# Performance work log

Measured on AMD Instinct MI355X. Metric: run time of the kernel, lower is better.

Reference implementation:

```python
import jax, jax.numpy as jnp
import numpy as np

EMBED_DIM = 768
HEADS = 8
HEAD_DIM = 128  # gnn_hidden_dim
OUT_DIM = HEADS * HEAD_DIM  # 1024, concat=True
NEG_SLOPE = 0.2  # PyG GATConv leaky_relu slope


def setup_inputs() -> dict:
    key = jax.random.key(0)
    ks = jax.random.split(key, 12)
    N, E = 10000, 160000
    x = jax.random.normal(ks[0], (N, EMBED_DIM), dtype=jnp.float32)
    edge_index = jax.random.randint(ks[1], (2, E), 0, N, dtype=jnp.int32)
    edge_attr = jax.random.uniform(ks[2], (E, 1), dtype=jnp.float32)
    # GATConv params (single layer, edge_dim=1)
    sc = 1.0 / np.sqrt(EMBED_DIM)
    W = jax.random.normal(ks[3], (EMBED_DIM, OUT_DIM), dtype=jnp.float32) * sc
    att_src = jax.random.normal(ks[4], (HEADS, HEAD_DIM), dtype=jnp.float32) * 0.1
    att_dst = jax.random.normal(ks[5], (HEADS, HEAD_DIM), dtype=jnp.float32) * 0.1
    W_edge = jax.random.normal(ks[6], (1, OUT_DIM), dtype=jnp.float32)
    att_edge = jax.random.normal(ks[7], (HEADS, HEAD_DIM), dtype=jnp.float32) * 0.1
    bias = jnp.zeros((OUT_DIM,), dtype=jnp.float32)
    # final classifier: in = 3*OUT_DIM (global pool + text node + image node)
    clf_W = jax.random.normal(ks[8], (3 * OUT_DIM, 2), dtype=jnp.float32) * (1.0 / np.sqrt(3 * OUT_DIM))
    clf_b = jnp.zeros((2,), dtype=jnp.float32)
    return {
        'x': x, 'edge_index': edge_index, 'edge_attr': edge_attr,
        'text_idx': 0, 'image_idx': 1,
        'W': W, 'att_src': att_src, 'att_dst': att_dst,
        'W_edge': W_edge, 'att_edge': att_edge, 'bias': bias,
        'clf_W': clf_W, 'clf_b': clf_b,
    }


def gat_layer(x, edge_index, edge_attr, W, att_src, att_dst, W_edge, att_edge, bias):
    N = x.shape[0]
    # add self-loops with edge_attr = mean of existing edge_attr (PyG default fill_value='mean')
    loop = jnp.arange(N, dtype=edge_index.dtype)
    ei = jnp.concatenate([edge_index, jnp.stack([loop, loop])], axis=1)
    ea_mean = jnp.mean(edge_attr, axis=0, keepdims=True)
    ea = jnp.concatenate([edge_attr, jnp.broadcast_to(ea_mean, (N, edge_attr.shape[1]))], axis=0)
    src, dst = ei[0], ei[1]
    xs = (x @ W).reshape(N, HEADS, HEAD_DIM)             # [N, H, C]
    a_src = jnp.einsum('nhc,hc->nh', xs, att_src)        # per-node src logits
    a_dst = jnp.einsum('nhc,hc->nh', xs, att_dst)
    e_emb = (ea @ W_edge).reshape(-1, HEADS, HEAD_DIM)   # [Etot, H, C]
    a_edge = jnp.einsum('ehc,hc->eh', e_emb, att_edge)
    alpha = jax.nn.leaky_relu(a_src[src] + a_dst[dst] + a_edge, NEG_SLOPE)  # [Etot, H]
    # softmax over incoming edges of each dst node
    m = jax.ops.segment_max(alpha, dst, num_segments=N)
    ex = jnp.exp(alpha - m[dst])
    denom = jax.ops.segment_sum(ex, dst, num_segments=N)
    w = ex / denom[dst]                                  # normalized attention [Etot, H]
    msg = xs[src] * w[:, :, None]                        # [Etot, H, C]
    out = jax.ops.segment_sum(msg, dst, num_segments=N)  # [N, H, C]
    return out.reshape(N, OUT_DIM) + bias


def reference(x, edge_index, edge_attr, text_idx, image_idx,
              W, att_src, att_dst, W_edge, att_edge, bias, clf_W, clf_b):
    # single GAT layer (num_gat_layers=1 -> no ELU/dropout after, eval mode)
    h = gat_layer(x, edge_index, edge_attr, W, att_src, att_dst, W_edge, att_edge, bias)
    g = jnp.mean(h, axis=0, keepdims=True)               # global_mean_pool, batch=None
    t = h[text_idx][None, :]
    im = h[image_idx][None, :]
    fused = jnp.concatenate([g, t, im], axis=1)          # [1, 3*OUT_DIM]
    logits = fused @ clf_W + clf_b                       # [1, 2]
    return logits
```

## Files before the change

### kernel.cpp

```cpp
#include <hip/hip_runtime.h>

#define NN 10000
#define EE 160000
#define ETOT (EE + NN)
#define EMB 768
#define ODIM 1024
#define NEG 0.2f
#define CAP 56

#define OFF_P      0
#define OFF_Q      12288
#define OFF_EAACC  12296
#define OFF_CNTD   12304
#define OFF_CNTS   22304
#define ZERO_START 12296
#define ZERO_CNT   20008
#define OFF_A      32304
#define OFF_SRCD   192304
#define OFF_DSTS   752304
#define OFF_PACK   1312304
#define OFF_EXD    1482304
#define OFF_EXS    5962304
#define OFF_RDEN   10442304
#define OFF_S      10522304
#define OFF_Z      10602304
#define OFF_YPART  10614592

__global__ __launch_bounds__(256) void k1f(
    const float* __restrict__ W, const float* __restrict__ att_src,
    const float* __restrict__ att_dst, const float* __restrict__ W_edge,
    const float* __restrict__ att_edge, const float* __restrict__ edge_attr,
    const int* __restrict__ ei, float* __restrict__ ws) {
  int b = blockIdx.x;
  if (b < 48) {
    int tid = b * 256 + threadIdx.x;
    int k = tid >> 4, j = tid & 15, h = j & 7;
    const float* att = (j < 8) ? att_src : att_dst;
    const float* wp = W + k * ODIM + h * 128;
    const float* ap = att + h * 128;
    float acc = 0.f;
    #pragma unroll 8
    for (int c = 0; c < 128; ++c) acc += wp[c] * ap[c];
    ws[OFF_P + k * 16 + j] = acc;
  } else if (b == 48) {
    if (threadIdx.x < 8) {
      int h = threadIdx.x;
      float acc = 0.f;
      #pragma unroll 8
      for (int c = 0; c < 128; ++c) acc += W_edge[h * 128 + c] * att_edge[h * 128 + c];
      ws[OFF_Q + h] = acc;
    }
  } else if (b < 113) {
    int bi = b - 49;
    float acc = 0.f;
    for (int i = bi * 256 + threadIdx.x; i < EE; i += 64 * 256) acc += edge_attr[i];
    #pragma unroll
    for (int off = 32; off > 0; off >>= 1) acc += __shfl_down(acc, off, 64);
    if ((threadIdx.x & 63) == 0) atomicAdd(&ws[OFF_EAACC], acc);
  } else {
    int e = (b - 113) * 256 + threadIdx.x;
    if (e >= ETOT) return;
    int src, dst;
    if (e < EE) { src = ei[e]; dst = ei[EE + e]; } else { src = dst = e - EE; }
    int* cntd = (int*)(ws + OFF_CNTD);
    int* cnts = (int*)(ws + OFF_CNTS);
    int pd = atomicAdd(&cntd[dst], 1);
    if (pd < CAP) ((int*)(ws + OFF_SRCD))[dst * CAP + pd] = src;
    int ps = atomicAdd(&cnts[src], 1);
    if (ps < CAP) ((int*)(ws + OFF_DSTS))[src * CAP + ps] = dst;
    if (pd > CAP) pd = CAP;
    if (ps > CAP) ps = CAP;
    ((int*)(ws + OFF_PACK))[e] = pd | (ps << 16);
  }
}

__global__ __launch_bounds__(256) void kAx(const float* __restrict__ x,
                                           float* __restrict__ ws) {
  __shared__ float smem[12288];
  for (int i = threadIdx.x; i < 3072; i += 256)
    ((float4*)smem)[i] = ((const float4*)(ws + OFF_P))[i];
  __syncthreads();
  int nl = threadIdx.x & 31, cg = threadIdx.x >> 5;
  int n = blockIdx.x * 32 + nl;
  float a[16];
  #pragma unroll
  for (int j = 0; j < 16; ++j) a[j] = 0.f;
  if (n < NN) {
    const float4* xr = (const float4*)(x + n * EMB + cg * 96);
    for (int kk = 0; kk < 24; ++kk) {
      float4 xv = xr[kk];
      const float* pr = &smem[(cg * 96 + kk * 4) * 16];
      #pragma unroll
      for (int j = 0; j < 16; ++j) a[j] += xv.x * pr[j];
      #pragma unroll
      for (int j = 0; j < 16; ++j) a[j] += xv.y * pr[16 + j];
      #pragma unroll
      for (int j = 0; j < 16; ++j) a[j] += xv.z * pr[32 + j];
      #pragma unroll
      for (int j = 0; j < 16; ++j) a[j] += xv.w * pr[48 + j];
    }
  }
  __syncthreads();
  #pragma unroll
  for (int j = 0; j < 16; ++j) smem[(cg * 16 + j) * 33 + nl] = a[j];
  __syncthreads();
  for (int w = threadIdx.x; w < 512; w += 256) {
    int rnl = w >> 4, j = w & 15;
    int nn = blockIdx.x * 32 + rnl;
    if (nn < NN) {
      float s = 0.f;
      #pragma unroll
      for (int c2 = 0; c2 < 8; ++c2) s += smem[(c2 * 16 + j) * 33 + rnl];
      ws[OFF_A + nn * 16 + j] = s;
    }
  }
}

__global__ __launch_bounds__(128) void kE(const int* __restrict__ ei,
                                          const float* __restrict__ edge_attr,
                                          const float* __restrict__ bias,
                                          const float* __restrict__ clf_W,
                                          const float* __restrict__ clf_b,
                                          float* __restrict__ out,
                                          float* __restrict__ ws) {
  __shared__ float red[4];
  int* wsI = (int*)ws;
  if (blockIdx.x < 1329) {
    int e = blockIdx.x * 128 + threadIdx.x;
    if (e >= ETOT) return;
    int src, dst; float ea;
    if (e < EE) { src = ei[e]; dst = ei[EE + e]; ea = edge_attr[e]; }
    else { src = dst = e - EE; ea = ws[OFF_EAACC] * (1.0f / EE); }
    int pk = wsI[OFF_PACK + e];
    int pd = pk & 0xffff, ps = pk >> 16;
    const float4* as4 = (const float4*)(ws + OFF_A + src * 16);
    const float4* ad4 = (const float4*)(ws + OFF_A + dst * 16 + 8);
    float4 s0 = as4[0], s1 = as4[1], d0 = ad4[0], d1 = ad4[1];
    float asr[8] = {s0.x, s0.y, s0.z, s0.w, s1.x, s1.y, s1.z, s1.w};
    float ads[8] = {d0.x, d0.y, d0.z, d0.w, d1.x, d1.y, d1.z, d1.w};
    float ex[8];
    #pragma unroll
    for (int h = 0; h < 8; ++h) {
      float v = asr[h] + ads[h] + ea * ws[OFF_Q + h];
      v = (v >= 0.f) ? v : NEG * v;
      ex[h] = __expf(v);
    }
    float4 e0 = make_float4(ex[0], ex[1], ex[2], ex[3]);
    float4 e1 = make_float4(ex[4], ex[5], ex[6], ex[7]);
    if (pd < CAP) {
      float4* p = (float4*)(ws + OFF_EXD + (dst * CAP + pd) * 8);
      p[0] = e0; p[1] = e1;
    }
    if (ps < CAP) {
      float4* p = (float4*)(ws + OFF_EXS + (src * CAP + ps) * 8);
      p[0] = e0; p[1] = e1;
    }
  } else {
    int t = threadIdx.x;
    float b0 = 0.f, b1 = 0.f;
    for (int i = t; i < 3072; i += 128) {
      float f = bias[i & 1023];
      b0 += f * clf_W[2 * i];
      b1 += f * clf_W[2 * i + 1];
    }
    #pragma unroll
    for (int o = 32; o > 0; o >>= 1) {
      b0 += __shfl_down(b0, o, 64);
      b1 += __shfl_down(b1, o, 64);
    }
    if ((t & 63) == 0) { red[(t >> 6) * 2] = b0; red[(t >> 6) * 2 + 1] = b1; }
    __syncthreads();
    if (t == 0) {
      out[0] = clf_b[0] + red[0] + red[2];
      out[1] = clf_b[1] + red[1] + red[3];
    }
  }
}

__global__ __launch_bounds__(128) void kD(float* __restrict__ ws) {
  int t = blockIdx.x * 128 + threadIdx.x;
  int dst = t >> 3, h = t & 7;
  int deg = ((const int*)(ws + OFF_CNTD))[dst];
  if (deg > CAP) deg = CAP;
  const float* base = ws + OFF_EXD + dst * (CAP * 8) + h;
  float den = 0.f;
  for (int j = 0; j < deg; ++j) den += base[j * 8];
  ws[OFF_RDEN + t] = 1.0f / den;
}

__global__ __launch_bounds__(128) void kSZ(const float* __restrict__ x,
                                           const int* __restrict__ tptr,
                                           const int* __restrict__ iptr,
                                           float* __restrict__ ws) {
  __shared__ float sm[512];
  if (blockIdx.x < 625) {
    int t = blockIdx.x * 128 + threadIdx.x;
    int src = t >> 3, h = t & 7;
    int deg = ((const int*)(ws + OFF_CNTS))[src];
    if (deg > CAP) deg = CAP;
    const int* dstrow = (const int*)(ws + OFF_DSTS) + src * CAP;
    const float* exrow = ws + OFF_EXS + src * (CAP * 8) + h;
    float s = 0.f;
    for (int j = 0; j < deg; ++j)
      s += exrow[j * 8] * ws[OFF_RDEN + dstrow[j] * 8 + h];
    ws[OFF_S + t] = s;
  } else {
    float* wL = sm;
    int* srcS = (int*)(sm + 448);
    int* degP = (int*)(sm + 508);
    int r = blockIdx.x - 625;
    int d = r / 6, kc = r % 6;
    int target = (d == 0) ? tptr[0] : iptr[0];
    if (threadIdx.x == 0) {
      int dg = ((const int*)(ws + OFF_CNTD))[target];
      degP[0] = (dg > CAP) ? CAP : dg;
    }
    __syncthreads();
    int deg = degP[0];
    for (int idx = threadIdx.x; idx < deg * 8; idx += 128) {
      int j = idx >> 3, h = idx & 7;
      wL[idx] = ws[OFF_EXD + (target * CAP + j) * 8 + h]
              * ws[OFF_RDEN + target * 8 + h];
      if (h == 0) srcS[j] = ((const int*)(ws + OFF_SRCD))[target * CAP + j];
    }
    __syncthreads();
    int col = kc * 128 + threadIdx.x;
    float acc[8];
    #pragma unroll
    for (int h = 0; h < 8; ++h) acc[h] = 0.f;
    for (int j = 0; j < deg; ++j) {
      float xv = x[srcS[j] * EMB + col];
      const float* wv = &wL[j * 8];
      #pragma unroll
      for (int h = 0; h < 8; ++h) acc[h] += wv[h] * xv;
    }
    #pragma unroll
    for (int h = 0; h < 8; ++h) ws[OFF_Z + (d * 8 + h) * EMB + col] = acc[h];
  }
}

__global__ __launch_bounds__(256) void k7s(const float* __restrict__ x,
                                           float* __restrict__ ws) {
  __shared__ float sL[64 * 8];
  int base = blockIdx.x * 64;
  int c = blockIdx.y;
  for (int i = threadIdx.x; i < 512; i += 256) {
    int n = base + (i >> 3);
    sL[i] = (n < NN) ? ws[OFF_S + base * 8 + i] : 0.f;
  }
  __syncthreads();
  int col = c * 256 + threadIdx.x;
  float acc[8];
  #pragma unroll
  for (int h = 0; h < 8; ++h) acc[h] = 0.f;
  int nmax = (NN - base < 64) ? (NN - base) : 64;
  for (int i = 0; i < nmax; ++i) {
    float xv = x[(base + i) * EMB + col];
    const float* sv = &sL[i * 8];
    #pragma unroll
    for (int h = 0; h < 8; ++h) acc[h] += xv * sv[h];
  }
  float* yp = ws + OFF_YPART + blockIdx.x * 6144 + col;
  #pragma unroll
  for (int h = 0; h < 8; ++h) yp[h * 768] = acc[h];
}

__global__ __launch_bounds__(128) void k8(const float* __restrict__ W,
                                          const float* __restrict__ clf_W,
                                          float* __restrict__ out,
                                          float* __restrict__ ws) {
  __shared__ float vL[144];
  __shared__ float red[4];
  int h = blockIdx.x, kc = blockIdx.y, kbase = kc * 48;
  for (int i = threadIdx.x; i < 144; i += 128) {
    int d = i / 48, k = i - d * 48;
    float v;
    if (d == 0) {
      float acc = 0.f;
      for (int b = 0; b < 157; ++b)
        acc += ws[OFF_YPART + b * 6144 + h * 768 + kbase + k];
      v = acc * (1.0f / NN);
    } else {
      v = ws[OFF_Z + ((d - 1) * 8 + h) * 768 + kbase + k];
    }
    vL[i] = v;
  }
  __syncthreads();
  int c = threadIdx.x;
  float a0 = 0.f, a1 = 0.f, a2 = 0.f;
  #pragma unroll 4
  for (int k = 0; k < 48; ++k) {
    float wv = W[(kbase + k) * ODIM + h * 128 + c];
    a0 += vL[k] * wv;
    a1 += vL[48 + k] * wv;
    a2 += vL[96 + k] * wv;
  }
  int ib = h * 128 + c;
  float l0 = a0 * clf_W[2 * ib] + a1 * clf_W[2 * (1024 + ib)]
           + a2 * clf_W[2 * (2048 + ib)];
  float l1 = a0 * clf_W[2 * ib + 1] + a1 * clf_W[2 * (1024 + ib) + 1]
           + a2 * clf_W[2 * (2048 + ib) + 1];
  #pragma unroll
  for (int o = 32; o > 0; o >>= 1) {
    l0 += __shfl_down(l0, o, 64);
    l1 += __shfl_down(l1, o, 64);
  }
  if ((threadIdx.x & 63) == 0) {
    red[(threadIdx.x >> 6) * 2] = l0;
    red[(threadIdx.x >> 6) * 2 + 1] = l1;
  }
  __syncthreads();
  if (threadIdx.x == 0) {
    atomicAdd(&out[0], red[0] + red[2]);
    atomicAdd(&out[1], red[1] + red[3]);
  }
}

extern "C" void kernel_launch(void* const* d_in, const int* in_sizes, int n_in,
                              void* d_out, int out_size, void* d_ws, size_t ws_size,
                              hipStream_t stream) {
  const float* x        = (const float*)d_in[0];
  const int*   ei       = (const int*)d_in[1];
  const float* edge_attr= (const float*)d_in[2];
  const int*   tptr     = (const int*)d_in[3];
  const int*   iptr     = (const int*)d_in[4];
  const float* W        = (const float*)d_in[5];
  const float* att_src  = (const float*)d_in[6];
  const float* att_dst  = (const float*)d_in[7];
  const float* W_edge   = (const float*)d_in[8];
  const float* att_edge = (const float*)d_in[9];
  const float* bias     = (const float*)d_in[10];
  const float* clf_W    = (const float*)d_in[11];
  const float* clf_b    = (const float*)d_in[12];
  float* ws  = (float*)d_ws;
  float* out = (float*)d_out;

  hipMemsetAsync(ws + ZERO_START, 0, ZERO_CNT * sizeof(float), stream);
  k1f<<<778, 256, 0, stream>>>(W, att_src, att_dst, W_edge, att_edge, edge_attr, ei, ws);
  kAx<<<313, 256, 0, stream>>>(x, ws);
  kE<<<1330, 128, 0, stream>>>(ei, edge_attr, bias, clf_W, clf_b, out, ws);
  kD<<<625, 128, 0, stream>>>(ws);
  kSZ<<<637, 128, 0, stream>>>(x, tptr, iptr, ws);
  dim3 g7(157, 3);
  k7s<<<g7, 256, 0, stream>>>(x, ws);
  dim3 g8(8, 16);
  k8<<<g8, 128, 0, stream>>>(W, clf_W, out, ws);
}
```

Measured before the change: 194.1 us.

## Recompute attention exponentials on the fly and fuse per-source sums with x-projection

Drops the per-edge exponential kernel and its large EXD/EXS buffers. The CSR build now stores edge attributes alongside the indices, and the softmax numerators are recomputed from the per-node logits inside the denominator kernel and the source-sum kernel. The source-weight computation is fused into the x-weighted reduction kernel, and the bias/classifier init moves into the first kernel. This removes two launches and heavy intermediate traffic, in exchange for duplicating exp computation (three times per edge across the three column blocks) and more gathered loads.

```diff
diff --git a/kernel.cpp b/kernel.cpp
--- a/kernel.cpp
+++ b/kernel.cpp
@@ -17,30 +17,35 @@
 #define ZERO_CNT   20008
 #define OFF_A      32304
 #define OFF_SRCD   192304
-#define OFF_DSTS   752304
-#define OFF_PACK   1312304
-#define OFF_EXD    1482304
-#define OFF_EXS    5962304
-#define OFF_RDEN   10442304
-#define OFF_S      10522304
-#define OFF_Z      10602304
-#define OFF_YPART  10614592
+#define OFF_AED    752304
+#define OFF_DSTS   1312304
+#define OFF_AES    1872304
+#define OFF_RDEN   2432304
+#define OFF_Z      2512304
+#define OFF_YPART  2524592
+
+#define SELF_MARK 3.0e38f
 
 __global__ __launch_bounds__(256) void k1f(
     const float* __restrict__ W, const float* __restrict__ att_src,
     const float* __restrict__ att_dst, const float* __restrict__ W_edge,
     const float* __restrict__ att_edge, const float* __restrict__ edge_attr,
+    const float* __restrict__ bias, const float* __restrict__ clf_W,
+    const float* __restrict__ clf_b, float* __restrict__ out,
     const int* __restrict__ ei, float* __restrict__ ws) {
   int b = blockIdx.x;
   if (b < 48) {
     int tid = b * 256 + threadIdx.x;
     int k = tid >> 4, j = tid & 15, h = j & 7;
     const float* att = (j < 8) ? att_src : att_dst;
-    const float* wp = W + k * ODIM + h * 128;
-    const float* ap = att + h * 128;
+    const float4* wp = (const float4*)(W + k * ODIM + h * 128);
+    const float4* ap = (const float4*)(att + h * 128);
     float acc = 0.f;
     #pragma unroll 8
-    for (int c = 0; c < 128; ++c) acc += wp[c] * ap[c];
+    for (int c = 0; c < 32; ++c) {
+      float4 w4 = wp[c], a4 = ap[c];
+      acc += w4.x * a4.x + w4.y * a4.y + w4.z * a4.z + w4.w * a4.w;
+    }
     ws[OFF_P + k * 16 + j] = acc;
   } else if (b == 48) {
     if (threadIdx.x < 8) {
@@ -50,27 +55,51 @@
       for (int c = 0; c < 128; ++c) acc += W_edge[h * 128 + c] * att_edge[h * 128 + c];
       ws[OFF_Q + h] = acc;
     }
-  } else if (b < 113) {
-    int bi = b - 49;
+  } else if (b == 49) {
+    __shared__ float red[8];
+    int t = threadIdx.x;
+    float b0 = 0.f, b1 = 0.f;
+    for (int i = t; i < 3072; i += 256) {
+      float f = bias[i & 1023];
+      b0 += f * clf_W[2 * i];
+      b1 += f * clf_W[2 * i + 1];
+    }
+    #pragma unroll
+    for (int o = 32; o > 0; o >>= 1) {
+      b0 += __shfl_down(b0, o, 64);
+      b1 += __shfl_down(b1, o, 64);
+    }
+    if ((t & 63) == 0) { red[(t >> 6) * 2] = b0; red[(t >> 6) * 2 + 1] = b1; }
+    __syncthreads();
+    if (t == 0) {
+      out[0] = clf_b[0] + red[0] + red[2] + red[4] + red[6];
+      out[1] = clf_b[1] + red[1] + red[3] + red[5] + red[7];
+    }
+  } else if (b < 114) {
+    int bi = b - 50;
     float acc = 0.f;
     for (int i = bi * 256 + threadIdx.x; i < EE; i += 64 * 256) acc += edge_attr[i];
     #pragma unroll
     for (int off = 32; off > 0; off >>= 1) acc += __shfl_down(acc, off, 64);
     if ((threadIdx.x & 63) == 0) atomicAdd(&ws[OFF_EAACC], acc);
   } else {
-    int e = (b - 113) * 256 + threadIdx.x;
+    int e = (b - 114) * 256 + threadIdx.x;
     if (e >= ETOT) return;
-    int src, dst;
-    if (e < EE) { src = ei[e]; dst = ei[EE + e]; } else { src = dst = e - EE; }
+    int src, dst; float ea;
+    if (e < EE) { src = ei[e]; dst = ei[EE + e]; ea = edge_attr[e]; }
+    else { src = dst = e - EE; ea = SELF_MARK; }
     int* cntd = (int*)(ws + OFF_CNTD);
     int* cnts = (int*)(ws + OFF_CNTS);
     int pd = atomicAdd(&cntd[dst], 1);
-    if (pd < CAP) ((int*)(ws + OFF_SRCD))[dst * CAP + pd] = src;
+    if (pd < CAP) {
+      ((int*)(ws + OFF_SRCD))[dst * CAP + pd] = src;
+      ws[OFF_AED + dst * CAP + pd] = ea;
+    }
     int ps = atomicAdd(&cnts[src], 1);
-    if (ps < CAP) ((int*)(ws + OFF_DSTS))[src * CAP + ps] = dst;
-    if (pd > CAP) pd = CAP;
-    if (ps > CAP) ps = CAP;
-    ((int*)(ws + OFF_PACK))[e] = pd | (ps << 16);
+    if (ps < CAP) {
+      ((int*)(ws + OFF_DSTS))[src * CAP + ps] = dst;
+      ws[OFF_AES + src * CAP + ps] = ea;
+    }
   }
 }
 
@@ -116,153 +145,104 @@
   }
 }
 
-__global__ __launch_bounds__(128) void kE(const int* __restrict__ ei,
-                                          const float* __restrict__ edge_attr,
-                                          const float* __restrict__ bias,
-                                          const float* __restrict__ clf_W,
-                                          const float* __restrict__ clf_b,
-                                          float* __restrict__ out,
-                                          float* __restrict__ ws) {
-  __shared__ float red[4];
-  int* wsI = (int*)ws;
-  if (blockIdx.x < 1329) {
-    int e = blockIdx.x * 128 + threadIdx.x;
-    if (e >= ETOT) return;
-    int src, dst; float ea;
-    if (e < EE) { src = ei[e]; dst = ei[EE + e]; ea = edge_attr[e]; }
-    else { src = dst = e - EE; ea = ws[OFF_EAACC] * (1.0f / EE); }
-    int pk = wsI[OFF_PACK + e];
-    int pd = pk & 0xffff, ps = pk >> 16;
-    const float4* as4 = (const float4*)(ws + OFF_A + src * 16);
-    const float4* ad4 = (const float4*)(ws + OFF_A + dst * 16 + 8);
-    float4 s0 = as4[0], s1 = as4[1], d0 = ad4[0], d1 = ad4[1];
-    float asr[8] = {s0.x, s0.y, s0.z, s0.w, s1.x, s1.y, s1.z, s1.w};
-    float ads[8] = {d0.x, d0.y, d0.z, d0.w, d1.x, d1.y, d1.z, d1.w};
-    float ex[8];
-    #pragma unroll
-    for (int h = 0; h < 8; ++h) {
-      float v = asr[h] + ads[h] + ea * ws[OFF_Q + h];
-      v = (v >= 0.f) ? v : NEG * v;
-      ex[h] = __expf(v);
-    }
-    float4 e0 = make_float4(ex[0], ex[1], ex[2], ex[3]);
-    float4 e1 = make_float4(ex[4], ex[5], ex[6], ex[7]);
-    if (pd < CAP) {
-      float4* p = (float4*)(ws + OFF_EXD + (dst * CAP + pd) * 8);
-      p[0] = e0; p[1] = e1;
-    }
-    if (ps < CAP) {
-      float4* p = (float4*)(ws + OFF_EXS + (src * CAP + ps) * 8);
-      p[0] = e0; p[1] = e1;
-    }
-  } else {
-    int t = threadIdx.x;
-    float b0 = 0.f, b1 = 0.f;
-    for (int i = t; i < 3072; i += 128) {
-      float f = bias[i & 1023];
-      b0 += f * clf_W[2 * i];
-      b1 += f * clf_W[2 * i + 1];
-    }
-    #pragma unroll
-    for (int o = 32; o > 0; o >>= 1) {
-      b0 += __shfl_down(b0, o, 64);
-      b1 += __shfl_down(b1, o, 64);
-    }
-    if ((t & 63) == 0) { red[(t >> 6) * 2] = b0; red[(t >> 6) * 2 + 1] = b1; }
-    __syncthreads();
-    if (t == 0) {
-      out[0] = clf_b[0] + red[0] + red[2];
-      out[1] = clf_b[1] + red[1] + red[3];
-    }
-  }
-}
-
 __global__ __launch_bounds__(128) void kD(float* __restrict__ ws) {
   int t = blockIdx.x * 128 + threadIdx.x;
   int dst = t >> 3, h = t & 7;
   int deg = ((const int*)(ws + OFF_CNTD))[dst];
   if (deg > CAP) deg = CAP;
-  const float* base = ws + OFF_EXD + dst * (CAP * 8) + h;
+  float adh = ws[OFF_A + dst * 16 + 8 + h];
+  float qh = ws[OFF_Q + h];
+  float mean = ws[OFF_EAACC] * (1.0f / EE);
+  const int* srow = (const int*)(ws + OFF_SRCD) + dst * CAP;
+  const float* aerow = ws + OFF_AED + dst * CAP;
   float den = 0.f;
-  for (int j = 0; j < deg; ++j) den += base[j * 8];
+  for (int j = 0; j < deg; ++j) {
+    float ae = aerow[j];
+    if (ae > 1e37f) ae = mean;
+    float v = ws[OFF_A + srow[j] * 16 + h] + adh + ae * qh;
+    v = (v >= 0.f) ? v : NEG * v;
+    den += __expf(v);
+  }
   ws[OFF_RDEN + t] = 1.0f / den;
 }
 
-__global__ __launch_bounds__(128) void kSZ(const float* __restrict__ x,
-                                           const int* __restrict__ tptr,
-                                           const int* __restrict__ iptr,
-                                           float* __restrict__ ws) {
-  __shared__ float sm[512];
-  if (blockIdx.x < 625) {
-    int t = blockIdx.x * 128 + threadIdx.x;
-    int src = t >> 3, h = t & 7;
-    int deg = ((const int*)(ws + OFF_CNTS))[src];
+__global__ __launch_bounds__(256) void kSYZ(const float* __restrict__ x,
+                                            const int* __restrict__ tptr,
+                                            const int* __restrict__ iptr,
+                                            float* __restrict__ ws) {
+  __shared__ float sL[512];
+  __shared__ int srcS[CAP];
+  float mean = ws[OFF_EAACC] * (1.0f / EE);
+  if (blockIdx.x < 471) {
+    int bx = blockIdx.x / 3, c = blockIdx.x % 3;
+    int base = bx * 64;
+    for (int t = threadIdx.x; t < 512; t += 256) {
+      int n = base + (t >> 3), h = t & 7;
+      float s = 0.f;
+      if (n < NN) {
+        int deg = ((const int*)(ws + OFF_CNTS))[n];
+        if (deg > CAP) deg = CAP;
+        float ash = ws[OFF_A + n * 16 + h];
+        float qh = ws[OFF_Q + h];
+        const int* drow = (const int*)(ws + OFF_DSTS) + n * CAP;
+        const float* aerow = ws + OFF_AES + n * CAP;
+        for (int j = 0; j < deg; ++j) {
+          int dd = drow[j];
+          float ae = aerow[j];
+          if (ae > 1e37f) ae = mean;
+          float v = ash + ws[OFF_A + dd * 16 + 8 + h] + ae * qh;
+          v = (v >= 0.f) ? v : NEG * v;
+          s += __expf(v) * ws[OFF_RDEN + dd * 8 + h];
+        }
+      }
+      sL[t] = s;
+    }
+    __syncthreads();
+    int col = c * 256 + threadIdx.x;
+    float acc[8];
+    #pragma unroll
+    for (int h = 0; h < 8; ++h) acc[h] = 0.f;
+    int nmax = (NN - base < 64) ? (NN - base) : 64;
+    for (int i = 0; i < nmax; ++i) {
+      float xv = x[(base + i) * EMB + col];
+      const float* sv = &sL[i * 8];
+      #pragma unroll
+      for (int h = 0; h < 8; ++h) acc[h] += xv * sv[h];
+    }
+    float* yp = ws + OFF_YPART + bx * 6144 + col;
+    #pragma unroll
+    for (int h = 0; h < 8; ++h) yp[h * 768] = acc[h];
+  } else {
+    int r = blockIdx.x - 471;
+    int d = r / 3, kc = r % 3;
+    int target = (d == 0) ? tptr[0] : iptr[0];
+    int deg = ((const int*)(ws + OFF_CNTD))[target];
     if (deg > CAP) deg = CAP;
-    const int* dstrow = (const int*)(ws + OFF_DSTS) + src * CAP;
-    const float* exrow = ws + OFF_EXS + src * (CAP * 8) + h;
-    float s = 0.f;
-    for (int j = 0; j < deg; ++j)
-      s += exrow[j * 8] * ws[OFF_RDEN + dstrow[j] * 8 + h];
-    ws[OFF_S + t] = s;
-  } else {
-    float* wL = sm;
-    int* srcS = (int*)(sm + 448);
-    int* degP = (int*)(sm + 508);
-    int r = blockIdx.x - 625;
-    int d = r / 6, kc = r % 6;
-    int target = (d == 0) ? tptr[0] : iptr[0];
-    if (threadIdx.x == 0) {
-      int dg = ((const int*)(ws + OFF_CNTD))[target];
-      degP[0] = (dg > CAP) ? CAP : dg;
+    for (int idx = threadIdx.x; idx < deg * 8; idx += 256) {
+      int j = idx >> 3, h = idx & 7;
+      int srcj = ((const int*)(ws + OFF_SRCD))[target * CAP + j];
+      float ae = ws[OFF_AED + target * CAP + j];
+      if (ae > 1e37f) ae = mean;
+      float v = ws[OFF_A + srcj * 16 + h] + ws[OFF_A + target * 16 + 8 + h]
+              + ae * ws[OFF_Q + h];
+      v = (v >= 0.f) ? v : NEG * v;
+      sL[idx] = __expf(v) * ws[OFF_RDEN + target * 8 + h];
+      if (h == 0) srcS[j] = srcj;
     }
     __syncthreads();
-    int deg = degP[0];
-    for (int idx = threadIdx.x; idx < deg * 8; idx += 128) {
-      int j = idx >> 3, h = idx & 7;
-      wL[idx] = ws[OFF_EXD + (target * CAP + j) * 8 + h]
-              * ws[OFF_RDEN + target * 8 + h];
-      if (h == 0) srcS[j] = ((const int*)(ws + OFF_SRCD))[target * CAP + j];
-    }
-    __syncthreads();
-    int col = kc * 128 + threadIdx.x;
+    int col = kc * 256 + threadIdx.x;
     float acc[8];
     #pragma unroll
     for (int h = 0; h < 8; ++h) acc[h] = 0.f;
     for (int j = 0; j < deg; ++j) {
       float xv = x[srcS[j] * EMB + col];
-      const float* wv = &wL[j * 8];
+      const float* wv = &sL[j * 8];
       #pragma unroll
       for (int h = 0; h < 8; ++h) acc[h] += wv[h] * xv;
     }
     #pragma unroll
     for (int h = 0; h < 8; ++h) ws[OFF_Z + (d * 8 + h) * EMB + col] = acc[h];
   }
-}
-
-__global__ __launch_bounds__(256) void k7s(const float* __restrict__ x,
-                                           float* __restrict__ ws) {
-  __shared__ float sL[64 * 8];
-  int base = blockIdx.x * 64;
-  int c = blockIdx.y;
-  for (int i = threadIdx.x; i < 512; i += 256) {
-    int n = base + (i >> 3);
-    sL[i] = (n < NN) ? ws[OFF_S + base * 8 + i] : 0.f;
-  }
-  __syncthreads();
-  int col = c * 256 + threadIdx.x;
-  float acc[8];
-  #pragma unroll
-  for (int h = 0; h < 8; ++h) acc[h] = 0.f;
-  int nmax = (NN - base < 64) ? (NN - base) : 64;
-  for (int i = 0; i < nmax; ++i) {
-    float xv = x[(base + i) * EMB + col];
-    const float* sv = &sL[i * 8];
-    #pragma unroll
-    for (int h = 0; h < 8; ++h) acc[h] += xv * sv[h];
-  }
-  float* yp = ws + OFF_YPART + blockIdx.x * 6144 + col;
-  #pragma unroll
-  for (int h = 0; h < 8; ++h) yp[h * 768] = acc[h];
 }
 
 __global__ __launch_bounds__(128) void k8(const float* __restrict__ W,
@@ -336,13 +316,11 @@
   float* out = (float*)d_out;
 
   hipMemsetAsync(ws + ZERO_START, 0, ZERO_CNT * sizeof(float), stream);
-  k1f<<<778, 256, 0, stream>>>(W, att_src, att_dst, W_edge, att_edge, edge_attr, ei, ws);
+  k1f<<<779, 256, 0, stream>>>(W, att_src, att_dst, W_edge, att_edge, edge_attr,
+                               bias, clf_W, clf_b, out, ei, ws);
   kAx<<<313, 256, 0, stream>>>(x, ws);
-  kE<<<1330, 128, 0, stream>>>(ei, edge_attr, bias, clf_W, clf_b, out, ws);
   kD<<<625, 128, 0, stream>>>(ws);
-  kSZ<<<637, 128, 0, stream>>>(x, tptr, iptr, ws);
-  dim3 g7(157, 3);
-  k7s<<<g7, 256, 0, stream>>>(x, ws);
+  kSYZ<<<477, 256, 0, stream>>>(x, tptr, iptr, ws);
   dim3 g8(8, 16);
   k8<<<g8, 128, 0, stream>>>(W, clf_W, out, ws);
 }
```

Measured after the change: 192.8 us. No clear change (-0.7%).
